# Kernel optimization log

Hardware: AMD Instinct MI355X
Metric: run time of the kernel (lower is better)

## Reference

```python
import jax, jax.numpy as jnp
import numpy as np

N = 100000        # nodes
E = 1600000       # edges (avg degree 16)
F_IN = 512        # num_features
H1, D1 = 8, 8     # layer-1 heads x per-head dim (concat -> 64)
C = 16            # num_classes (layer-2: 1 head, dim C)
NEG_SLOPE = 0.2


def setup_inputs() -> dict:
    key = jax.random.key(0)
    ks = jax.random.split(key, 8)
    x = jax.random.normal(ks[0], (N, F_IN), dtype=jnp.float32)
    edge_index = jax.random.randint(ks[1], (2, E), 0, N, dtype=jnp.int64)
    W1 = jax.random.normal(ks[2], (F_IN, H1 * D1), dtype=jnp.float32) / np.float32(np.sqrt(F_IN))
    a1_src = jax.random.normal(ks[3], (H1, D1), dtype=jnp.float32) * 0.1
    a1_dst = jax.random.normal(ks[4], (H1, D1), dtype=jnp.float32) * 0.1
    W2 = jax.random.normal(ks[5], (H1 * D1, C), dtype=jnp.float32) / np.float32(np.sqrt(H1 * D1))
    a2_src = jax.random.normal(ks[6], (1, C), dtype=jnp.float32) * 0.1
    a2_dst = jax.random.normal(ks[7], (1, C), dtype=jnp.float32) * 0.1
    return {"x": x, "edge_index": edge_index, "W1": W1, "a1_src": a1_src,
            "a1_dst": a1_dst, "W2": W2, "a2_src": a2_src, "a2_dst": a2_dst}


def gat_layer(x, src, dst, W, a_s, a_d, heads, out_dim):
    """Multi-head GAT conv: gather -> per-edge leaky-relu score -> segment
    softmax over destination -> scatter-aggregate. Returns [N, heads, out_dim]."""
    n = x.shape[0]
    h = (x @ W).reshape(n, heads, out_dim)            # [N, H, D]
    es = jnp.einsum('nhd,hd->nh', h, a_s)             # source attention term
    ed = jnp.einsum('nhd,hd->nh', h, a_d)             # dest attention term
    e = jax.nn.leaky_relu(es[src] + ed[dst], NEG_SLOPE)   # [E, H]
    m = jax.ops.segment_max(e, dst, num_segments=n)       # stable softmax max
    ex = jnp.exp(e - m[dst])
    s = jax.ops.segment_sum(ex, dst, num_segments=n)
    alpha = ex / s[dst]                               # [E, H]
    out = jax.ops.segment_sum(h[src] * alpha[..., None], dst, num_segments=n)
    return out                                        # [N, H, D]


def reference(x, edge_index, W1, a1_src, a1_dst, W2, a2_src, a2_dst):
    n = x.shape[0]
    loop = jnp.arange(n, dtype=edge_index.dtype)
    src = jnp.concatenate([edge_index[0], loop])      # add self-loops
    dst = jnp.concatenate([edge_index[1], loop])
    # eval mode: dropout(p=0.6, training=False) is identity
    h1 = gat_layer(x, src, dst, W1, a1_src, a1_dst, H1, D1).reshape(n, H1 * D1)
    h1 = jax.nn.elu(h1)
    h2 = gat_layer(h1, src, dst, W2, a2_src, a2_dst, 1, C).reshape(n, C)
    return jax.nn.log_softmax(h2, axis=1)
```

## Files before the change

### kernel.cpp

```cpp
#include <hip/hip_runtime.h>
#include <hip/hip_bf16.h>

#define F_IN 512
#define H1 8
#define D1 8
#define F_MID 64
#define C 16
#define NEG_SLOPE 0.2f
#define BIN_CHUNK 4096
#define NB_MAX 1024
#define BUCKET_SHIFT 7
#define BUCKET_STRIDE 3072
#define SRC_BITS 17
#define SRC_MASK ((1 << SRC_BITS) - 1)

typedef __attribute__((ext_vector_type(8))) short bf16x8;
typedef __attribute__((ext_vector_type(4))) float f32x4;

static __device__ __forceinline__ unsigned short f2bf(float f) {
    __hip_bfloat16 h = __float2bfloat16(f);
    return *(unsigned short*)&h;
}

__global__ __launch_bounds__(256) void k_bin_w1t(const int* __restrict__ src,
                                                 const int* __restrict__ dst,
                                                 int* __restrict__ gcur,
                                                 int* __restrict__ bucketed,
                                                 const float* __restrict__ W1,
                                                 __hip_bfloat16* __restrict__ w1t,
                                                 int n_edges, int nb, int nbin) {
    const int t = threadIdx.x;
    if ((int)blockIdx.x >= nbin) {
        int idx = ((int)blockIdx.x - nbin) * 256 + t;
        int k = idx >> 6, n = idx & 63;
        w1t[n * F_IN + k] = __float2bfloat16(W1[idx]);
        return;
    }
    __shared__ int cnt[NB_MAX];
    __shared__ int base[NB_MAX];
    const int eb = blockIdx.x * BIN_CHUNK;
    int dc[BIN_CHUNK / 256];
#pragma unroll
    for (int i = 0; i < BIN_CHUNK / 256; ++i) {
        int e = eb + i * 256 + t;
        dc[i] = (e < n_edges) ? dst[e] : -1;
    }
    for (int b = t; b < nb; b += 256) cnt[b] = 0;
    __syncthreads();
#pragma unroll
    for (int i = 0; i < BIN_CHUNK / 256; ++i)
        if (dc[i] >= 0) atomicAdd(&cnt[dc[i] >> BUCKET_SHIFT], 1);
    __syncthreads();
    for (int b = t; b < nb; b += 256) {
        int c = cnt[b];
        base[b] = c > 0 ? atomicAdd(&gcur[b], c) : 0;
        cnt[b] = 0;
    }
    __syncthreads();
#pragma unroll
    for (int i = 0; i < BIN_CHUNK / 256; ++i) {
        if (dc[i] >= 0) {
            int e = eb + i * 256 + t;
            int d = dc[i];
            int b = d >> BUCKET_SHIFT;
            int local = atomicAdd(&cnt[b], 1);
            bucketed[(size_t)b * BUCKET_STRIDE + base[b] + local] =
                ((d & ((1 << BUCKET_SHIFT) - 1)) << SRC_BITS) | src[e];
        }
    }
}

__global__ __launch_bounds__(256) void k_gemm1_place(const float* __restrict__ x,
                                                     const __hip_bfloat16* __restrict__ w1t,
                                                     const float* __restrict__ a1s,
                                                     const float* __restrict__ a1d,
                                                     __hip_bfloat16* __restrict__ h1b,
                                                     float* __restrict__ es1,
                                                     float* __restrict__ ed1,
                                                     const int* __restrict__ gcur,
                                                     const int* __restrict__ bucketed,
                                                     int* __restrict__ row_start,
                                                     int* __restrict__ sorted_src,
                                                     int n_nodes, int n_edges, int ngemm) {
    __shared__ int stage[BUCKET_STRIDE];
    __shared__ int cnt[1 << BUCKET_SHIFT];
    __shared__ int cur[1 << BUCKET_SHIFT];
    __shared__ int wsum[4];
    const int t = threadIdx.x;

    if ((int)blockIdx.x < ngemm) {
        const int wv = t >> 6, l = t & 63;
        const int q = l >> 4, m16 = l & 15;
        const int rowbase = blockIdx.x * 64;

        const int node = rowbase + wv * 16 + m16;
        const int gx = node < n_nodes ? node : n_nodes - 1;
        const float* xrow = x + (size_t)gx * F_IN;

        f32x4 acc[4];
#pragma unroll
        for (int i = 0; i < 4; ++i) acc[i] = (f32x4){0.f, 0.f, 0.f, 0.f};

        for (int kt = 0; kt < F_IN; kt += 64) {
#pragma unroll
            for (int kk = 0; kk < 2; ++kk) {
                const float* xp = xrow + kt + kk * 32 + q * 8;
                float4 v0 = *(const float4*)(xp);
                float4 v1 = *(const float4*)(xp + 4);
                ushort4 b0, b1;
                b0.x = f2bf(v0.x); b0.y = f2bf(v0.y); b0.z = f2bf(v0.z); b0.w = f2bf(v0.w);
                b1.x = f2bf(v1.x); b1.y = f2bf(v1.y); b1.z = f2bf(v1.z); b1.w = f2bf(v1.w);
                union { ushort4 u4[2]; bf16x8 v8; } bu;
                bu.u4[0] = b0; bu.u4[1] = b1;
                const bf16x8 bfrag = bu.v8;
#pragma unroll
                for (int tn = 0; tn < 4; ++tn) {
                    bf16x8 afrag = *(const bf16x8*)(w1t + (size_t)(tn * 16 + m16) * F_IN
                                                    + kt + kk * 32 + q * 8);
                    acc[tn] = __builtin_amdgcn_mfma_f32_16x16x32_bf16(afrag, bfrag, acc[tn], 0, 0, 0);
                }
            }
        }

        const bool ok = node < n_nodes;
#pragma unroll
        for (int tn = 0; tn < 4; ++tn) {
            const f32x4 a = acc[tn];
            const int nw0 = tn * 16 + q * 4;
            float vs = a.x * a1s[nw0] + a.y * a1s[nw0 + 1] + a.z * a1s[nw0 + 2] + a.w * a1s[nw0 + 3];
            float vd = a.x * a1d[nw0] + a.y * a1d[nw0 + 1] + a.z * a1d[nw0 + 2] + a.w * a1d[nw0 + 3];
            vs += __shfl_xor(vs, 16, 64);
            vd += __shfl_xor(vd, 16, 64);
            if (ok) {
                ushort4 b;
                b.x = f2bf(a.x); b.y = f2bf(a.y); b.z = f2bf(a.z); b.w = f2bf(a.w);
                *(ushort4*)(h1b + (size_t)node * F_MID + nw0) = b;
                if ((q & 1) == 0) {
                    const int head = 2 * tn + (q >> 1);
                    es1[node * H1 + head] = vs;
                    ed1[node * H1 + head] = vd;
                }
            }
        }
        return;
    }

    const int b = (int)blockIdx.x - ngemm;
    if (t < (1 << BUCKET_SHIFT)) cnt[t] = 0;
    int pre = 0;
    for (int j = t; j < b; j += 256) pre += gcur[j];
#pragma unroll
    for (int off = 1; off < 64; off <<= 1) pre += __shfl_xor(pre, off, 64);
    if ((t & 63) == 0) wsum[t >> 6] = pre;
    __syncthreads();
    const int base0 = wsum[0] + wsum[1] + wsum[2] + wsum[3];
    if (b == 0 && t == 0) row_start[n_nodes] = n_edges;

    const int total = gcur[b];
    const int* bp = bucketed + (size_t)b * BUCKET_STRIDE;
    for (int i = t; i < total; i += 256) {
        int e = bp[i];
        stage[i] = e;
        atomicAdd(&cnt[e >> SRC_BITS], 1);
    }
    __syncthreads();
    if (t < (1 << BUCKET_SHIFT)) cur[t] = cnt[t];
    __syncthreads();
#pragma unroll
    for (int d = 1; d < (1 << BUCKET_SHIFT); d <<= 1) {
        int u = 0;
        if (t < (1 << BUCKET_SHIFT) && t >= d) u = cur[t - d];
        __syncthreads();
        if (t < (1 << BUCKET_SHIFT)) cur[t] += u;
        __syncthreads();
    }
    if (t < (1 << BUCKET_SHIFT)) {
        int node = (b << BUCKET_SHIFT) + t;
        int excl = cur[t] - cnt[t];
        if (node < n_nodes) row_start[node] = base0 + excl;
        cur[t] = excl;
    }
    __syncthreads();
    for (int i = t; i < total; i += 256) {
        int e = stage[i];
        int p = atomicAdd(&cur[e >> SRC_BITS], 1);
        sorted_src[base0 + p] = e & SRC_MASK;
    }
}

__global__ __launch_bounds__(256) void k_gather1(const int* __restrict__ row_start,
                                                 const int* __restrict__ sorted_src,
                                                 const __hip_bfloat16* __restrict__ h1b,
                                                 const float* __restrict__ es1,
                                                 const float* __restrict__ ed1,
                                                 __hip_bfloat16* __restrict__ h1c, int n_nodes) {
    const int n = blockIdx.x * 4 + (threadIdx.x >> 6);
    if (n >= n_nodes) return;
    const int lane = threadIdx.x & 63;
    const int h = lane >> 3;
    const float edh = ed1[n * H1 + h];
    const int beg = row_start[n], end = row_start[n + 1];
    float acc = 0.f, den = 0.f;
    for (int base = beg; base < end; base += 64) {
        const int m = min(64, end - base);
        const int li = lane < m ? lane : (m - 1);
        const int myS = sorted_src[base + li];
        int j = 0;
        for (; j + 8 <= m; j += 8) {
            const int s0 = __shfl(myS, j, 64),     s1 = __shfl(myS, j + 1, 64);
            const int s2 = __shfl(myS, j + 2, 64), s3 = __shfl(myS, j + 3, 64);
            const int s4 = __shfl(myS, j + 4, 64), s5 = __shfl(myS, j + 5, 64);
            const int s6 = __shfl(myS, j + 6, 64), s7 = __shfl(myS, j + 7, 64);
            float e0 = es1[s0 * H1 + h], e1 = es1[s1 * H1 + h];
            float e2 = es1[s2 * H1 + h], e3 = es1[s3 * H1 + h];
            float e4 = es1[s4 * H1 + h], e5 = es1[s5 * H1 + h];
            float e6 = es1[s6 * H1 + h], e7 = es1[s7 * H1 + h];
            const float f0 = __bfloat162float(h1b[(size_t)s0 * F_MID + lane]);
            const float f1 = __bfloat162float(h1b[(size_t)s1 * F_MID + lane]);
            const float f2 = __bfloat162float(h1b[(size_t)s2 * F_MID + lane]);
            const float f3 = __bfloat162float(h1b[(size_t)s3 * F_MID + lane]);
            const float f4 = __bfloat162float(h1b[(size_t)s4 * F_MID + lane]);
            const float f5 = __bfloat162float(h1b[(size_t)s5 * F_MID + lane]);
            const float f6 = __bfloat162float(h1b[(size_t)s6 * F_MID + lane]);
            const float f7 = __bfloat162float(h1b[(size_t)s7 * F_MID + lane]);
            e0 += edh; e1 += edh; e2 += edh; e3 += edh;
            e4 += edh; e5 += edh; e6 += edh; e7 += edh;
            e0 = e0 > 0.f ? e0 : NEG_SLOPE * e0;
            e1 = e1 > 0.f ? e1 : NEG_SLOPE * e1;
            e2 = e2 > 0.f ? e2 : NEG_SLOPE * e2;
            e3 = e3 > 0.f ? e3 : NEG_SLOPE * e3;
            e4 = e4 > 0.f ? e4 : NEG_SLOPE * e4;
            e5 = e5 > 0.f ? e5 : NEG_SLOPE * e5;
            e6 = e6 > 0.f ? e6 : NEG_SLOPE * e6;
            e7 = e7 > 0.f ? e7 : NEG_SLOPE * e7;
            const float w0 = __expf(e0), w1 = __expf(e1), w2 = __expf(e2), w3 = __expf(e3);
            const float w4 = __expf(e4), w5 = __expf(e5), w6 = __expf(e6), w7 = __expf(e7);
            acc += (w0 * f0 + w1 * f1 + w2 * f2 + w3 * f3)
                 + (w4 * f4 + w5 * f5 + w6 * f6 + w7 * f7);
            den += ((w0 + w1) + (w2 + w3)) + ((w4 + w5) + (w6 + w7));
        }
        for (; j + 4 <= m; j += 4) {
            const int s0 = __shfl(myS, j, 64), s1 = __shfl(myS, j + 1, 64);
            const int s2 = __shfl(myS, j + 2, 64), s3 = __shfl(myS, j + 3, 64);
            float e0 = es1[s0 * H1 + h], e1 = es1[s1 * H1 + h];
            float e2 = es1[s2 * H1 + h], e3 = es1[s3 * H1 + h];
            const float f0 = __bfloat162float(h1b[(size_t)s0 * F_MID + lane]);
            const float f1 = __bfloat162float(h1b[(size_t)s1 * F_MID + lane]);
            const float f2 = __bfloat162float(h1b[(size_t)s2 * F_MID + lane]);
            const float f3 = __bfloat162float(h1b[(size_t)s3 * F_MID + lane]);
            e0 += edh; e1 += edh; e2 += edh; e3 += edh;
            e0 = e0 > 0.f ? e0 : NEG_SLOPE * e0;
            e1 = e1 > 0.f ? e1 : NEG_SLOPE * e1;
            e2 = e2 > 0.f ? e2 : NEG_SLOPE * e2;
            e3 = e3 > 0.f ? e3 : NEG_SLOPE * e3;
            const float w0 = __expf(e0), w1 = __expf(e1), w2 = __expf(e2), w3 = __expf(e3);
            acc += w0 * f0 + w1 * f1 + w2 * f2 + w3 * f3;
            den += (w0 + w1) + (w2 + w3);
        }
        for (; j < m; ++j) {
            const int s = __shfl(myS, j, 64);
            float ev = es1[s * H1 + h] + edh;
            ev = ev > 0.f ? ev : NEG_SLOPE * ev;
            const float w = __expf(ev);
            acc += w * __bfloat162float(h1b[(size_t)s * F_MID + lane]);
            den += w;
        }
    }
    float evs = es1[n * H1 + h] + edh;
    evs = evs > 0.f ? evs : NEG_SLOPE * evs;
    const float ws = __expf(evs);
    acc += ws * __bfloat162float(h1b[(size_t)n * F_MID + lane]);
    den += ws;
    float v = acc / den;
    v = v > 0.f ? v : expm1f(v);
    h1c[(size_t)n * F_MID + lane] = __float2bfloat16(v);
}

__global__ void k_gemm2(const __hip_bfloat16* __restrict__ h1c, const float* __restrict__ W2,
                        const float* __restrict__ a2s, const float* __restrict__ a2d,
                        __hip_bfloat16* __restrict__ h2b, float* __restrict__ es2,
                        float* __restrict__ ed2, int n_nodes) {
    __shared__ float w2s[F_MID * C];
    __shared__ float h1s[16][F_MID + 1];
    const int t = threadIdx.x;
    const int nb = blockIdx.x * 16;
    for (int i = t; i < F_MID * C; i += 256) w2s[i] = W2[i];
    {
        int r = t >> 4, k4 = (t & 15) << 2;
        int n = nb + r;
        const __hip_bfloat16* p = h1c + (size_t)(n < n_nodes ? n : n_nodes - 1) * F_MID + k4;
        ushort4 v = *(const ushort4*)p;
        h1s[r][k4 + 0] = __bfloat162float(*(const __hip_bfloat16*)&v.x);
        h1s[r][k4 + 1] = __bfloat162float(*(const __hip_bfloat16*)&v.y);
        h1s[r][k4 + 2] = __bfloat162float(*(const __hip_bfloat16*)&v.z);
        h1s[r][k4 + 3] = __bfloat162float(*(const __hip_bfloat16*)&v.w);
    }
    __syncthreads();
    const int r = t >> 4, c = t & 15;
    const int n = nb + r;
    float acc = 0.f;
#pragma unroll
    for (int k = 0; k < F_MID; ++k) acc += h1s[r][k] * w2s[k * C + c];
    float vs = acc * a2s[c], vd = acc * a2d[c];
#pragma unroll
    for (int off = 1; off < 16; off <<= 1) {
        vs += __shfl_xor(vs, off, 64);
        vd += __shfl_xor(vd, off, 64);
    }
    if (n < n_nodes) {
        h2b[(size_t)n * C + c] = __float2bfloat16(acc);
        if (c == 0) { es2[n] = vs; ed2[n] = vd; }
    }
}

__global__ __launch_bounds__(256) void k_gather2(const int* __restrict__ row_start,
                                                 const int* __restrict__ sorted_src,
                                                 const __hip_bfloat16* __restrict__ h2b,
                                                 const float* __restrict__ es2,
                                                 const float* __restrict__ ed2,
                                                 float* __restrict__ out, int n_nodes) {
    const int n = blockIdx.x * 16 + (threadIdx.x >> 4);
    if (n >= n_nodes) return;
    const int lane = threadIdx.x & 63;
    const int c = lane & 15;
    const int g = lane >> 4;
    const float ed = ed2[n];
    const int beg = row_start[n], end = row_start[n + 1];
    float acc = 0.f, den = 0.f;
    for (int base = beg; base < end; base += 16) {
        const int m = min(16, end - base);
        const int li = c < m ? c : (m - 1);
        const int myS = sorted_src[base + li];
        float evp = es2[myS] + ed;
        evp = evp > 0.f ? evp : NEG_SLOPE * evp;
        const float wli = __expf(evp);
        int j = 0;
        for (; j + 4 <= m; j += 4) {
            const int s0 = __shfl(myS, g * 16 + j, 64), s1 = __shfl(myS, g * 16 + j + 1, 64);
            const int s2 = __shfl(myS, g * 16 + j + 2, 64), s3 = __shfl(myS, g * 16 + j + 3, 64);
            const float w0 = __shfl(wli, g * 16 + j, 64), w1 = __shfl(wli, g * 16 + j + 1, 64);
            const float w2 = __shfl(wli, g * 16 + j + 2, 64), w3 = __shfl(wli, g * 16 + j + 3, 64);
            const float f0 = __bfloat162float(h2b[(size_t)s0 * C + c]);
            const float f1 = __bfloat162float(h2b[(size_t)s1 * C + c]);
            const float f2 = __bfloat162float(h2b[(size_t)s2 * C + c]);
            const float f3 = __bfloat162float(h2b[(size_t)s3 * C + c]);
            acc += w0 * f0 + w1 * f1 + w2 * f2 + w3 * f3;
            den += (w0 + w1) + (w2 + w3);
        }
        for (; j < m; ++j) {
            const int s = __shfl(myS, g * 16 + j, 64);
            const float w = __shfl(wli, g * 16 + j, 64);
            acc += w * __bfloat162float(h2b[(size_t)s * C + c]);
            den += w;
        }
    }
    float evs = es2[n] + ed;
    evs = evs > 0.f ? evs : NEG_SLOPE * evs;
    const float ws = __expf(evs);
    acc += ws * __bfloat162float(h2b[(size_t)n * C + c]);
    den += ws;
    const float v = acc / den;
    float mx = v;
#pragma unroll
    for (int off = 1; off < 16; off <<= 1) mx = fmaxf(mx, __shfl_xor(mx, off, 64));
    float se = __expf(v - mx);
#pragma unroll
    for (int off = 1; off < 16; off <<= 1) se += __shfl_xor(se, off, 64);
    out[(size_t)n * C + c] = v - mx - __logf(se);
}

extern "C" void kernel_launch(void* const* d_in, const int* in_sizes, int n_in,
                              void* d_out, int out_size, void* d_ws, size_t ws_size,
                              hipStream_t stream) {
    const float* x   = (const float*)d_in[0];
    const int*   ei  = (const int*)d_in[1];
    const float* W1  = (const float*)d_in[2];
    const float* a1s = (const float*)d_in[3];
    const float* a1d = (const float*)d_in[4];
    const float* W2  = (const float*)d_in[5];
    const float* a2s = (const float*)d_in[6];
    const float* a2d = (const float*)d_in[7];
    float* out = (float*)d_out;

    const int n_nodes = in_sizes[0] / F_IN;
    const int n_edges = in_sizes[1] / 2;
    const int* src = ei;
    const int* dst = ei + n_edges;
    const int nb = (n_nodes + (1 << BUCKET_SHIFT) - 1) >> BUCKET_SHIFT;
    const int nbin = (n_edges + BIN_CHUNK - 1) / BIN_CHUNK;
    const int ngemm = (n_nodes + 63) / 64;

    float* fws = (float*)d_ws;
    float* es1 = fws;
    float* ed1 = es1 + (size_t)n_nodes * H1;
    float* es2 = ed1 + (size_t)n_nodes * H1;
    float* ed2 = es2 + n_nodes;
    __hip_bfloat16* h1b = (__hip_bfloat16*)(ed2 + n_nodes);
    __hip_bfloat16* h2b = h1b + (size_t)n_nodes * F_MID;
    __hip_bfloat16* h1c = h2b + (size_t)n_nodes * C;
    __hip_bfloat16* w1t = h1c + (size_t)n_nodes * F_MID;
    int* iws         = (int*)(w1t + F_IN * F_MID);
    int* gcur        = iws;
    int* row_start   = gcur + NB_MAX;
    int* sorted_src  = row_start + n_nodes + 1;
    int* bucketed    = sorted_src + n_edges;

    hipMemsetAsync(gcur, 0, NB_MAX * sizeof(int), stream);

    k_bin_w1t<<<nbin + (F_IN * F_MID) / 256, 256, 0, stream>>>(src, dst, gcur, bucketed,
                                                               W1, w1t, n_edges, nb, nbin);

    k_gemm1_place<<<ngemm + nb, 256, 0, stream>>>(x, w1t, a1s, a1d, h1b, es1, ed1,
                                                  gcur, bucketed, row_start, sorted_src,
                                                  n_nodes, n_edges, ngemm);

    k_gather1<<<(n_nodes + 3) / 4, 256, 0, stream>>>(row_start, sorted_src, h1b, es1, ed1, h1c, n_nodes);

    k_gemm2<<<(n_nodes + 15) / 16, 256, 0, stream>>>(h1c, W2, a2s, a2d, h2b, es2, ed2, n_nodes);
    k_gather2<<<(n_nodes + 15) / 16, 256, 0, stream>>>(row_start, sorted_src, h2b, es2, ed2, out, n_nodes);
}
```

Before: 468.4 us.

## Stage binned edges in LDS for coalesced bucket and sorted_src writes

```diff
diff --git a/kernel.cpp b/kernel.cpp
--- a/kernel.cpp
+++ b/kernel.cpp
@@ -22,51 +22,88 @@
     return *(unsigned short*)&h;
 }
 
-__global__ __launch_bounds__(256) void k_bin_w1t(const int* __restrict__ src,
-                                                 const int* __restrict__ dst,
-                                                 int* __restrict__ gcur,
-                                                 int* __restrict__ bucketed,
-                                                 const float* __restrict__ W1,
-                                                 __hip_bfloat16* __restrict__ w1t,
-                                                 int n_edges, int nb, int nbin) {
+__global__ __launch_bounds__(256) void k_init(const float* __restrict__ W1,
+                                              __hip_bfloat16* __restrict__ w1t,
+                                              int* __restrict__ gcur) {
     const int t = threadIdx.x;
-    if ((int)blockIdx.x >= nbin) {
-        int idx = ((int)blockIdx.x - nbin) * 256 + t;
-        int k = idx >> 6, n = idx & 63;
-        w1t[n * F_IN + k] = __float2bfloat16(W1[idx]);
+    if ((int)blockIdx.x == (F_IN * F_MID) / 256) {
+        for (int i = t; i < NB_MAX; i += 256) gcur[i] = 0;
         return;
     }
+    int idx = blockIdx.x * 256 + t;
+    int k = idx >> 6, n = idx & 63;
+    w1t[n * F_IN + k] = __float2bfloat16(W1[idx]);
+}
+
+__global__ __launch_bounds__(256) void k_bin(const int* __restrict__ src,
+                                             const int* __restrict__ dst,
+                                             int* __restrict__ gcur,
+                                             int* __restrict__ bucketed,
+                                             int n_edges) {
     __shared__ int cnt[NB_MAX];
-    __shared__ int base[NB_MAX];
+    __shared__ int excl[NB_MAX];
+    __shared__ int gbase[NB_MAX];
+    __shared__ int curloc[NB_MAX];
+    __shared__ int stage[BIN_CHUNK];
+    __shared__ unsigned short sbkt[BIN_CHUNK];
+    __shared__ int wtot[4];
+    const int t = threadIdx.x;
+    const int lane = t & 63, w = t >> 6;
     const int eb = blockIdx.x * BIN_CHUNK;
+    const int ecnt = min(BIN_CHUNK, n_edges - eb);
+
     int dc[BIN_CHUNK / 256];
 #pragma unroll
     for (int i = 0; i < BIN_CHUNK / 256; ++i) {
         int e = eb + i * 256 + t;
         dc[i] = (e < n_edges) ? dst[e] : -1;
     }
-    for (int b = t; b < nb; b += 256) cnt[b] = 0;
+    for (int b = t; b < NB_MAX; b += 256) cnt[b] = 0;
     __syncthreads();
 #pragma unroll
     for (int i = 0; i < BIN_CHUNK / 256; ++i)
         if (dc[i] >= 0) atomicAdd(&cnt[dc[i] >> BUCKET_SHIFT], 1);
     __syncthreads();
-    for (int b = t; b < nb; b += 256) {
-        int c = cnt[b];
-        base[b] = c > 0 ? atomicAdd(&gcur[b], c) : 0;
-        cnt[b] = 0;
-    }
-    __syncthreads();
+
+    const int c0 = cnt[4 * t], c1 = cnt[4 * t + 1], c2 = cnt[4 * t + 2], c3 = cnt[4 * t + 3];
+    const int ls = c0 + c1 + c2 + c3;
+    int is = ls;
+#pragma unroll
+    for (int off = 1; off < 64; off <<= 1) {
+        int v = __shfl_up(is, off, 64);
+        if (lane >= off) is += v;
+    }
+    if (lane == 63) wtot[w] = is;
+    __syncthreads();
+    int woff = 0;
+#pragma unroll
+    for (int i = 0; i < 4; ++i) if (i < w) woff += wtot[i];
+    const int e0 = woff + is - ls;
+    excl[4 * t] = e0;               curloc[4 * t] = e0;
+    excl[4 * t + 1] = e0 + c0;      curloc[4 * t + 1] = e0 + c0;
+    excl[4 * t + 2] = e0 + c0 + c1; curloc[4 * t + 2] = e0 + c0 + c1;
+    excl[4 * t + 3] = e0 + c0 + c1 + c2; curloc[4 * t + 3] = e0 + c0 + c1 + c2;
+    gbase[4 * t]     = c0 > 0 ? atomicAdd(&gcur[4 * t], c0) : 0;
+    gbase[4 * t + 1] = c1 > 0 ? atomicAdd(&gcur[4 * t + 1], c1) : 0;
+    gbase[4 * t + 2] = c2 > 0 ? atomicAdd(&gcur[4 * t + 2], c2) : 0;
+    gbase[4 * t + 3] = c3 > 0 ? atomicAdd(&gcur[4 * t + 3], c3) : 0;
+    __syncthreads();
+
 #pragma unroll
     for (int i = 0; i < BIN_CHUNK / 256; ++i) {
         if (dc[i] >= 0) {
             int e = eb + i * 256 + t;
             int d = dc[i];
             int b = d >> BUCKET_SHIFT;
-            int local = atomicAdd(&cnt[b], 1);
-            bucketed[(size_t)b * BUCKET_STRIDE + base[b] + local] =
-                ((d & ((1 << BUCKET_SHIFT) - 1)) << SRC_BITS) | src[e];
-        }
+            int p = atomicAdd(&curloc[b], 1);
+            stage[p] = ((d & ((1 << BUCKET_SHIFT) - 1)) << SRC_BITS) | src[e];
+            sbkt[p] = (unsigned short)b;
+        }
+    }
+    __syncthreads();
+    for (int i = t; i < ecnt; i += 256) {
+        int b = sbkt[i];
+        bucketed[(size_t)b * BUCKET_STRIDE + gbase[b] + (i - excl[b])] = stage[i];
     }
 }
 
@@ -83,6 +120,7 @@
                                                      int* __restrict__ sorted_src,
                                                      int n_nodes, int n_edges, int ngemm) {
     __shared__ int stage[BUCKET_STRIDE];
+    __shared__ int sstage[BUCKET_STRIDE];
     __shared__ int cnt[1 << BUCKET_SHIFT];
     __shared__ int cur[1 << BUCKET_SHIFT];
     __shared__ int wsum[4];
@@ -184,8 +222,11 @@
     for (int i = t; i < total; i += 256) {
         int e = stage[i];
         int p = atomicAdd(&cur[e >> SRC_BITS], 1);
-        sorted_src[base0 + p] = e & SRC_MASK;
-    }
+        sstage[p] = e & SRC_MASK;
+    }
+    __syncthreads();
+    for (int i = t; i < total; i += 256)
+        sorted_src[base0 + i] = sstage[i];
 }
 
 __global__ __launch_bounds__(256) void k_gather1(const int* __restrict__ row_start,
@@ -405,10 +446,9 @@
     int* sorted_src  = row_start + n_nodes + 1;
     int* bucketed    = sorted_src + n_edges;
 
-    hipMemsetAsync(gcur, 0, NB_MAX * sizeof(int), stream);
-
-    k_bin_w1t<<<nbin + (F_IN * F_MID) / 256, 256, 0, stream>>>(src, dst, gcur, bucketed,
-                                                               W1, w1t, n_edges, nb, nbin);
+    k_init<<<(F_IN * F_MID) / 256 + 1, 256, 0, stream>>>(W1, w1t, gcur);
+
+    k_bin<<<nbin, 256, 0, stream>>>(src, dst, gcur, bucketed, n_edges);
 
     k_gemm1_place<<<ngemm + nb, 256, 0, stream>>>(x, w1t, a1s, a1d, h1b, es1, ed1,
                                                   gcur, bucketed, row_start, sorted_src,
```

New measurement: 478.2 us. +2.1%, slower.
